# Performance work log

Measured on AMD Instinct MI355X. Metric: run time of the kernel, lower is better.

The kernel has to match this reference:

```python
import jax, jax.numpy as jnp
import numpy as np

B, S, E, H = 4, 2048, 1024, 16
D = E // H
EPS = 1e-5
NEG = -1e9


def setup_inputs() -> dict:
    key = jax.random.key(0)
    ks = jax.random.split(key, 16)
    scale = 1.0 / np.sqrt(E)
    inp = {
        "q": jax.random.normal(ks[0], (B, S, E), jnp.float32),
        "k": jax.random.normal(ks[1], (B, S, E), jnp.float32),
        "v": jax.random.normal(ks[2], (B, S, E), jnp.float32),
        "mask": jax.random.randint(ks[3], (B, S, S), 0, 2).astype(bool),
        # Linear weights stored as (in, out); matches torch math with random init.
        "W1": jax.random.normal(ks[4], (E, E), jnp.float32) * scale,
        "b1": jnp.zeros((E,), jnp.float32),
        "W2": jax.random.normal(ks[5], (E, E), jnp.float32) * scale,
        "b2": jnp.zeros((E,), jnp.float32),
        "W3": jax.random.normal(ks[6], (E, E), jnp.float32) * scale,
        "b3": jnp.zeros((E,), jnp.float32),
        "W4": jax.random.normal(ks[7], (E, E), jnp.float32) * scale,
        "b4": jnp.zeros((E,), jnp.float32),
        "gamma": jnp.ones((E,), jnp.float32),
        "beta": jnp.zeros((E,), jnp.float32),
    }
    return inp


def _layer_norm(x, gamma, beta):
    mu = jnp.mean(x, axis=-1, keepdims=True)
    var = jnp.mean(jnp.square(x - mu), axis=-1, keepdims=True)
    return (x - mu) * jax.lax.rsqrt(var + EPS) * gamma + beta


def reference(q, k, v, mask, W1, b1, W2, b2, W3, b3, W4, b4, gamma, beta):
    vn = _layer_norm(v, gamma, beta)          # same LayerNorm params used twice
    residual = vn
    # projections -> [B, H, S, D]
    qh = (q @ W1 + b1).reshape(B, S, H, D).transpose(0, 2, 1, 3)
    kh = (k @ W2 + b2).reshape(B, S, H, D).transpose(0, 2, 1, 3)
    vh = (vn @ W3 + b3).reshape(B, S, H, D).transpose(0, 2, 1, 3)
    # NOTE: original module omits the 1/sqrt(D) scale -- keep it faithful.
    scores = jnp.einsum("bhqd,bhkd->bhqk", qh, kh)
    scores = jnp.where(mask[:, None, :, :], NEG, scores)
    attn = jax.nn.softmax(scores, axis=-1)
    out = jnp.einsum("bhqk,bhkd->bhqd", attn, vh)
    out = out.transpose(0, 2, 1, 3).reshape(B, S, E)
    out = out @ W4 + b4 + residual
    return _layer_norm(out, gamma, beta)
```

## Files before the change

### kernel.cpp

```cpp
#include <hip/hip_runtime.h>

typedef unsigned short u16;
typedef unsigned int u32;
typedef unsigned long long u64;
typedef float f32x4 __attribute__((ext_vector_type(4)));
typedef short short8 __attribute__((ext_vector_type(8)));
typedef short bf16x4 __attribute__((ext_vector_type(4)));

#define BB 4
#define SS 2048
#define EE 1024
#define HH 16
#define DD 64
#define EPSV 1e-5f
#define LOG2E 1.4426950408889634f

__device__ __forceinline__ u16 f2b(float x) {
  u32 u = __float_as_uint(x);
  u32 r = (u + 0x7fffu + ((u >> 16) & 1u)) >> 16;
  return (u16)r;
}
__device__ __forceinline__ float b2f(u16 u) {
  return __uint_as_float(((u32)u) << 16);
}
__device__ __forceinline__ u32 cvtpk(float lo, float hi) {
  u32 r;
  asm("v_cvt_pk_bf16_f32 %0, %1, %2" : "=v"(r) : "v"(lo), "v"(hi));
  return r;
}
__device__ __forceinline__ float fexp2(float x) {
  float r;
  asm("v_exp_f32 %0, %1" : "=v"(r) : "v"(x));
  return r;
}
__device__ __forceinline__ void gload16(const void* g, void* l) {
  __builtin_amdgcn_global_load_lds(
      (const __attribute__((address_space(1))) u32*)g,
      (__attribute__((address_space(3))) u32*)l, 16, 0, 0);
}
__device__ __forceinline__ f32x4 mfma16(bf16x4 a, bf16x4 b, f32x4 c) {
#if __has_builtin(__builtin_amdgcn_mfma_f32_16x16x16_bf16)
  return __builtin_amdgcn_mfma_f32_16x16x16_bf16(a, b, c, 0, 0, 0);
#elif __has_builtin(__builtin_amdgcn_mfma_f32_16x16x16bf16_1k)
  return __builtin_amdgcn_mfma_f32_16x16x16bf16_1k(a, b, c, 0, 0, 0);
#else
  asm("v_mfma_f32_16x16x16_bf16 %0, %1, %2, %3"
      : "=v"(c) : "v"(a), "v"(b), "v"(c));
  return c;
#endif
}

template<bool OUT_BF16>
__global__ __launch_bounds__(256) void ln_kernel(const float* __restrict__ x,
    const float* __restrict__ gamma, const float* __restrict__ beta,
    void* __restrict__ outp) {
  int row = blockIdx.x;
  int t = threadIdx.x;
  const float4* xr = (const float4*)(x + (size_t)row * EE);
  float4 v = xr[t];
  float s = v.x + v.y + v.z + v.w;
  #pragma unroll
  for (int o = 1; o < 64; o <<= 1) s += __shfl_xor(s, o);
  __shared__ float red[8];
  int wid = t >> 6;
  if ((t & 63) == 0) red[wid] = s;
  __syncthreads();
  float mean = (red[0] + red[1] + red[2] + red[3]) * (1.0f / EE);
  float d0 = v.x - mean, d1 = v.y - mean, d2 = v.z - mean, d3 = v.w - mean;
  float sq = d0 * d0 + d1 * d1 + d2 * d2 + d3 * d3;
  #pragma unroll
  for (int o = 1; o < 64; o <<= 1) sq += __shfl_xor(sq, o);
  if ((t & 63) == 0) red[4 + wid] = sq;
  __syncthreads();
  float var = (red[4] + red[5] + red[6] + red[7]) * (1.0f / EE);
  float rstd = rsqrtf(var + EPSV);
  float4 g = ((const float4*)gamma)[t];
  float4 be = ((const float4*)beta)[t];
  float o0 = d0 * rstd * g.x + be.x;
  float o1 = d1 * rstd * g.y + be.y;
  float o2 = d2 * rstd * g.z + be.z;
  float o3 = d3 * rstd * g.w + be.w;
  if (OUT_BF16) {
    ushort4 pk;
    pk.x = f2b(o0); pk.y = f2b(o1); pk.z = f2b(o2); pk.w = f2b(o3);
    *(ushort4*)((u16*)outp + (size_t)row * EE + t * 4) = pk;
  } else {
    ((float4*)((float*)outp + (size_t)row * EE))[t] = make_float4(o0, o1, o2, o3);
  }
}

__global__ __launch_bounds__(256) void pre_kernel(
    const float* __restrict__ v, const float* __restrict__ gamma,
    const float* __restrict__ beta, u16* __restrict__ vn,
    const float* __restrict__ q, u16* __restrict__ qbf,
    const float* __restrict__ k, u16* __restrict__ kbf,
    const int* __restrict__ mask, u64* __restrict__ mp,
    const float* __restrict__ W1, const float* __restrict__ W2,
    const float* __restrict__ W3, const float* __restrict__ W4,
    u16* __restrict__ W1t, u16* __restrict__ W2t,
    u16* __restrict__ W3t, u16* __restrict__ W4t) {
  __shared__ float tile[32][33];
  __shared__ float red[8];
  int idx = blockIdx.x;
  int t = threadIdx.x;
  if (idx < 8192) {
    int row = idx;
    float4 vv = ((const float4*)(v + (size_t)row * EE))[t];
    float s = vv.x + vv.y + vv.z + vv.w;
    #pragma unroll
    for (int o = 1; o < 64; o <<= 1) s += __shfl_xor(s, o);
    int wid = t >> 6;
    if ((t & 63) == 0) red[wid] = s;
    __syncthreads();
    float mean = (red[0] + red[1] + red[2] + red[3]) * (1.0f / EE);
    float d0 = vv.x - mean, d1 = vv.y - mean, d2 = vv.z - mean, d3 = vv.w - mean;
    float sq = d0 * d0 + d1 * d1 + d2 * d2 + d3 * d3;
    #pragma unroll
    for (int o = 1; o < 64; o <<= 1) sq += __shfl_xor(sq, o);
    if ((t & 63) == 0) red[4 + wid] = sq;
    __syncthreads();
    float var = (red[4] + red[5] + red[6] + red[7]) * (1.0f / EE);
    float rstd = rsqrtf(var + EPSV);
    float4 g = ((const float4*)gamma)[t];
    float4 be = ((const float4*)beta)[t];
    ushort4 pk;
    pk.x = f2b(d0 * rstd * g.x + be.x);
    pk.y = f2b(d1 * rstd * g.y + be.y);
    pk.z = f2b(d2 * rstd * g.z + be.z);
    pk.w = f2b(d3 * rstd * g.w + be.w);
    *(ushort4*)(vn + (size_t)row * EE + t * 4) = pk;
  } else if (idx < 16384) {
    int i = idx - 8192;
    const float* x = (i >= 4096) ? k : q;
    u16* y = (i >= 4096) ? kbf : qbf;
    size_t off = ((size_t)(i & 4095) * 256 + t) * 8;
    float4 a = *(const float4*)(x + off);
    float4 c = *(const float4*)(x + off + 4);
    uint4 pk;
    pk.x = (u32)f2b(a.x) | ((u32)f2b(a.y) << 16);
    pk.y = (u32)f2b(a.z) | ((u32)f2b(a.w) << 16);
    pk.z = (u32)f2b(c.x) | ((u32)f2b(c.y) << 16);
    pk.w = (u32)f2b(c.z) | ((u32)f2b(c.w) << 16);
    *(uint4*)(y + off) = pk;
  } else if (idx < 32768) {
    int widx = idx - 16384;
    int wv = t >> 6, lane = t & 63;
    size_t base = (size_t)widx * 1024 + wv * 256;
    int v0 = mask[base + 0 * 64 + lane];
    int v1 = mask[base + 1 * 64 + lane];
    int v2 = mask[base + 2 * 64 + lane];
    int v3 = mask[base + 3 * 64 + lane];
    u64 b0 = __ballot(v0 != 0);
    u64 b1 = __ballot(v1 != 0);
    u64 b2 = __ballot(v2 != 0);
    u64 b3 = __ballot(v3 != 0);
    if (lane == 0) {
      u64* dst = &mp[base >> 6];
      dst[0] = b0; dst[1] = b1; dst[2] = b2; dst[3] = b3;
    }
  } else {
    int s = idx - 32768;
    int w = s >> 10, t2 = s & 1023;
    int kb = (t2 & 31) * 32, nb = (t2 >> 5) * 32;
    const float* W = (w == 0) ? W1 : (w == 1) ? W2 : (w == 2) ? W3 : W4;
    u16* Wt = (w == 0) ? W1t : (w == 1) ? W2t : (w == 2) ? W3t : W4t;
    int r = t >> 3, c = (t & 7) * 4;
    float4 vv = *(const float4*)&W[(size_t)(kb + r) * EE + nb + c];
    tile[r][c] = vv.x; tile[r][c + 1] = vv.y;
    tile[r][c + 2] = vv.z; tile[r][c + 3] = vv.w;
    __syncthreads();
    uint2 val;
    val.x = (u32)f2b(tile[c][r]) | ((u32)f2b(tile[c + 1][r]) << 16);
    val.y = (u32)f2b(tile[c + 2][r]) | ((u32)f2b(tile[c + 3][r]) << 16);
    *(uint2*)&Wt[(size_t)(nb + r) * EE + kb + c] = val;
  }
}

__global__ __launch_bounds__(256) void gemm_proj(
    const u16* __restrict__ Aq, const u16* __restrict__ Ak,
    const u16* __restrict__ Av,
    const u16* __restrict__ W1t, const u16* __restrict__ W2t,
    const u16* __restrict__ W3t,
    const float* __restrict__ b1, const float* __restrict__ b2,
    const float* __restrict__ b3,
    u16* __restrict__ qh, u16* __restrict__ kh, u16* __restrict__ vt,
    int yoff) {
  constexpr int N = 1024, K = 1024;
  __shared__ u16 Al[128 * 32];
  __shared__ u16 Bl[128 * 32];
  int y = blockIdx.y + yoff;
  int sel = y >> 6, my = y & 63;
  const u16* Ap = (sel == 0) ? Aq : (sel == 1) ? Ak : Av;
  const u16* Bt = (sel == 0) ? W1t : (sel == 1) ? W2t : W3t;
  const float* bias = (sel == 0) ? b1 : (sel == 1) ? b2 : b3;
  u16* Cp = (sel == 0) ? qh : (sel == 1) ? kh : vt;
  float oscale = (sel == 0) ? LOG2E : 1.0f;

  int t = threadIdx.x;
  int lane = t & 63, wid = t >> 6;
  int mb = my * 128, nb = blockIdx.x * 128;
  int wm = (wid >> 1) * 64, wn = (wid & 1) * 64;
  int l15 = lane & 15, lg = lane >> 4;

  int srow = lane >> 2;
  int schunk = (lane & 3) ^ (srow & 3);
  const u16* Ag = Ap + (size_t)(mb + wid * 32 + srow) * K + schunk * 8;
  const u16* Bg = Bt + (size_t)(nb + wid * 32 + srow) * K + schunk * 8;
  u16* Alw0 = &Al[(wid * 32) * 32];
  u16* Alw1 = &Al[(wid * 32 + 16) * 32];
  u16* Blw0 = &Bl[(wid * 32) * 32];
  u16* Blw1 = &Bl[(wid * 32 + 16) * 32];
  int ca = (lg ^ (l15 & 3)) * 8;

  f32x4 acc[4][4] = {};
  for (int kt = 0; kt < K; kt += 32) {
    gload16(Ag + kt, Alw0);
    gload16(Ag + kt + (size_t)16 * K, Alw1);
    gload16(Bg + kt, Blw0);
    gload16(Bg + kt + (size_t)16 * K, Blw1);
    __syncthreads();
    short8 af[4], bfv[4];
    #pragma unroll
    for (int mf = 0; mf < 4; mf++)
      af[mf] = *(const short8*)&Al[(wm + mf * 16 + l15) * 32 + ca];
    #pragma unroll
    for (int nf = 0; nf < 4; nf++)
      bfv[nf] = *(const short8*)&Bl[(wn + nf * 16 + l15) * 32 + ca];
    #pragma unroll
    for (int mf = 0; mf < 4; mf++)
      #pragma unroll
      for (int nf = 0; nf < 4; nf++)
        acc[mf][nf] = __builtin_amdgcn_mfma_f32_16x16x32_bf16(af[mf], bfv[nf], acc[mf][nf], 0, 0, 0);
    __syncthreads();
  }
  float bv[4];
  #pragma unroll
  for (int nf = 0; nf < 4; nf++) bv[nf] = bias[nb + wn + nf * 16 + l15];
  if (sel == 2) {
    #pragma unroll
    for (int mf = 0; mf < 4; mf++) {
      int m0 = mb + wm + mf * 16 + lg * 4;
      int bq = m0 >> 11, s0 = m0 & 2047;
      #pragma unroll
      for (int nf = 0; nf < 4; nf++) {
        int n = nb + wn + nf * 16 + l15;
        int h = n >> 6, d = n & 63;
        ushort4 pk;
        pk.x = f2b(acc[mf][nf][0] + bv[nf]);
        pk.y = f2b(acc[mf][nf][1] + bv[nf]);
        pk.z = f2b(acc[mf][nf][2] + bv[nf]);
        pk.w = f2b(acc[mf][nf][3] + bv[nf]);
        *(ushort4*)&vt[((size_t)((bq * HH + h) * DD + d)) * SS + s0] = pk;
      }
    }
  } else {
    #pragma unroll
    for (int mf = 0; mf < 4; mf++) {
      #pragma unroll
      for (int r = 0; r < 4; r++) {
        int m = mb + wm + mf * 16 + lg * 4 + r;
        #pragma unroll
        for (int nf = 0; nf < 4; nf++) {
          int n = nb + wn + nf * 16 + l15;
          Cp[(size_t)m * N + n] = f2b((acc[mf][nf][r] + bv[nf]) * oscale);
        }
      }
    }
  }
}

__global__ __launch_bounds__(256) void gemm_out(const u16* __restrict__ Ap,
    const u16* __restrict__ Bt, const float* __restrict__ bias,
    const u16* __restrict__ resid, float* __restrict__ Cp) {
  constexpr int N = 1024, K = 1024;
  __shared__ u16 Al[128 * 32];
  __shared__ u16 Bl[128 * 32];
  int t = threadIdx.x;
  int lane = t & 63, wid = t >> 6;
  int mb = blockIdx.y * 128, nb = blockIdx.x * 128;
  int wm = (wid >> 1) * 64, wn = (wid & 1) * 64;
  int l15 = lane & 15, lg = lane >> 4;
  int srow = lane >> 2;
  int schunk = (lane & 3) ^ (srow & 3);
  const u16* Ag = Ap + (size_t)(mb + wid * 32 + srow) * K + schunk * 8;
  const u16* Bg = Bt + (size_t)(nb + wid * 32 + srow) * K + schunk * 8;
  u16* Alw0 = &Al[(wid * 32) * 32];
  u16* Alw1 = &Al[(wid * 32 + 16) * 32];
  u16* Blw0 = &Bl[(wid * 32) * 32];
  u16* Blw1 = &Bl[(wid * 32 + 16) * 32];
  int ca = (lg ^ (l15 & 3)) * 8;
  f32x4 acc[4][4] = {};
  for (int kt = 0; kt < K; kt += 32) {
    gload16(Ag + kt, Alw0);
    gload16(Ag + kt + (size_t)16 * K, Alw1);
    gload16(Bg + kt, Blw0);
    gload16(Bg + kt + (size_t)16 * K, Blw1);
    __syncthreads();
    short8 af[4], bfv[4];
    #pragma unroll
    for (int mf = 0; mf < 4; mf++)
      af[mf] = *(const short8*)&Al[(wm + mf * 16 + l15) * 32 + ca];
    #pragma unroll
    for (int nf = 0; nf < 4; nf++)
      bfv[nf] = *(const short8*)&Bl[(wn + nf * 16 + l15) * 32 + ca];
    #pragma unroll
    for (int mf = 0; mf < 4; mf++)
      #pragma unroll
      for (int nf = 0; nf < 4; nf++)
        acc[mf][nf] = __builtin_amdgcn_mfma_f32_16x16x32_bf16(af[mf], bfv[nf], acc[mf][nf], 0, 0, 0);
    __syncthreads();
  }
  float bv[4];
  #pragma unroll
  for (int nf = 0; nf < 4; nf++) bv[nf] = bias[nb + wn + nf * 16 + l15];
  #pragma unroll
  for (int mf = 0; mf < 4; mf++) {
    #pragma unroll
    for (int r = 0; r < 4; r++) {
      int m = mb + wm + mf * 16 + lg * 4 + r;
      #pragma unroll
      for (int nf = 0; nf < 4; nf++) {
        int n = nb + wn + nf * 16 + l15;
        float rv = b2f(resid[(size_t)m * N + n]);
        Cp[(size_t)m * N + n] = acc[mf][nf][r] + bv[nf] + rv;
      }
    }
  }
}

__global__ __launch_bounds__(256) void attn_kernel(const u16* __restrict__ qh,
    const u16* __restrict__ kh, const u16* __restrict__ vt,
    const u64* __restrict__ mp, u16* __restrict__ outp) {
  __shared__ u16 Kl[64 * 64];
  __shared__ u16 Vl[64 * 64];
  __shared__ u64 lutq[16];
  int t = threadIdx.x, lane = t & 63, wid = t >> 6;
  int bh = blockIdx.x, b = bh >> 4, h = bh & 15;
  int qt = blockIdx.y;
  int l15 = lane & 15, lg = lane >> 4;

  if (t < 16) {
    u32 n = t;
    u32 w0 = ((n & 1) ? 0u : 0xFFFFu) | ((n & 2) ? 0u : 0xFFFF0000u);
    u32 w1 = ((n & 4) ? 0u : 0xFFFFu) | ((n & 8) ? 0u : 0xFFFF0000u);
    lutq[n] = (u64)w0 | ((u64)w1 << 32);
  }

  int qrow0 = qt * 128 + wid * 16 + l15;
  int qrow1 = qrow0 + 64;
  const u16* qbase0 = qh + ((size_t)(b * SS + qrow0)) * EE + h * DD;
  const u16* qbase1 = qh + ((size_t)(b * SS + qrow1)) * EE + h * DD;
  short8 qa0 = *(const short8*)(qbase0 + lg * 8);
  short8 qa1 = *(const short8*)(qbase0 + 32 + lg * 8);
  short8 qb0 = *(const short8*)(qbase1 + lg * 8);
  short8 qb1 = *(const short8*)(qbase1 + 32 + lg * 8);
  const u64* mrow0 = mp + (size_t)(b * SS + qrow0) * (SS / 64);
  const u64* mrow1 = mp + (size_t)(b * SS + qrow1) * (SS / 64);

  bf16x4 onesv;
  #pragma unroll
  for (int i = 0; i < 4; i++) onesv[i] = (short)0x3F80;

  int r0 = wid * 16 + (lane >> 3);
  int r1 = r0 + 8;
  int cc = lane & 7;
  int wk0 = r0 * 64 + ((cc ^ (r0 & 7)) * 8);
  int wk1 = r1 * 64 + ((cc ^ (r1 & 7)) * 8);
  const u16* kgb = kh + ((size_t)b * SS) * EE + h * DD;
  const u16* vgb = vt + ((size_t)bh * DD) * SS;

  int ck0 = (lg ^ (l15 & 7)) * 8;
  int ck1 = ((4 + lg) ^ (l15 & 7)) * 8;
  int vbase0 = l15 * 64 + ((lg >> 1) ^ (l15 & 7)) * 8 + (lg & 1) * 4;

  f32x4 Oa[4] = {}, Ob[4] = {};
  f32x4 asuma = {}, asumb = {};
  constexpr int NT = SS / 64;

  uint4 sk0 = *(const uint4*)(kgb + (size_t)r0 * EE + cc * 8);
  uint4 sk1 = *(const uint4*)(kgb + (size_t)r1 * EE + cc * 8);
  uint4 sv0 = *(const uint4*)(vgb + (size_t)r0 * SS + cc * 8);
  uint4 sv1 = *(const uint4*)(vgb + (size_t)r1 * SS + cc * 8);
  const u16* kp0 = kgb + (size_t)(64 + r0) * EE + cc * 8;
  const u16* kp1 = kgb + (size_t)(64 + r1) * EE + cc * 8;
  const u16* vp0 = vgb + (size_t)r0 * SS + 64 + cc * 8;
  const u16* vp1 = vgb + (size_t)r1 * SS + 64 + cc * 8;
  u64 mwa = mrow0[0];
  u64 mwb = mrow1[0];

  for (int kt = 0; kt < NT; ++kt) {
    *(uint4*)&Kl[wk0] = sk0;
    *(uint4*)&Kl[wk1] = sk1;
    *(uint4*)&Vl[wk0] = sv0;
    *(uint4*)&Vl[wk1] = sv1;
    __syncthreads();

    sk0 = *(const uint4*)kp0; kp0 += 64 * EE;
    sk1 = *(const uint4*)kp1; kp1 += 64 * EE;
    sv0 = *(const uint4*)vp0; vp0 += 64;
    sv1 = *(const uint4*)vp1; vp1 += 64;
    u64 mwan = mrow0[kt + 1];
    u64 mwbn = mrow1[kt + 1];

    u32 mloa = (u32)(mwa >> (lg * 4));
    u32 mhia = (u32)(mwa >> 32 >> (lg * 4));
    u32 mlob = (u32)(mwb >> (lg * 4));
    u32 mhib = (u32)(mwb >> 32 >> (lg * 4));
    uint2 pata[4], patb[4];
    pata[0] = *(uint2*)&lutq[mloa & 15u];
    pata[1] = *(uint2*)&lutq[(mloa >> 16) & 15u];
    pata[2] = *(uint2*)&lutq[mhia & 15u];
    pata[3] = *(uint2*)&lutq[(mhia >> 16) & 15u];
    patb[0] = *(uint2*)&lutq[mlob & 15u];
    patb[1] = *(uint2*)&lutq[(mlob >> 16) & 15u];
    patb[2] = *(uint2*)&lutq[mhib & 15u];
    patb[3] = *(uint2*)&lutq[(mhib >> 16) & 15u];

    f32x4 sca[4], scb[4];
    #pragma unroll
    for (int nf = 0; nf < 4; nf++) {
      int row = nf * 16 + l15;
      short8 k0 = *(const short8*)&Kl[row * 64 + ck0];
      short8 k1 = *(const short8*)&Kl[row * 64 + ck1];
      f32x4 za = {}, zb = {};
      za = __builtin_amdgcn_mfma_f32_16x16x32_bf16(k0, qa0, za, 0, 0, 0);
      za = __builtin_amdgcn_mfma_f32_16x16x32_bf16(k1, qa1, za, 0, 0, 0);
      zb = __builtin_amdgcn_mfma_f32_16x16x32_bf16(k0, qb0, zb, 0, 0, 0);
      zb = __builtin_amdgcn_mfma_f32_16x16x32_bf16(k1, qb1, zb, 0, 0, 0);
      sca[nf] = za;
      scb[nf] = zb;
    }

    #pragma unroll
    for (int nf = 0; nf < 4; nf++) {
      #pragma unroll
      for (int r = 0; r < 4; r++) {
        sca[nf][r] = fexp2(sca[nf][r]);
        scb[nf][r] = fexp2(scb[nf][r]);
      }
    }

    #pragma unroll
    for (int nf = 0; nf < 4; nf++) {
      bf16x4 pba, pbb;
      ((u32*)&pba)[0] = cvtpk(sca[nf][0], sca[nf][1]) & pata[nf].x;
      ((u32*)&pba)[1] = cvtpk(sca[nf][2], sca[nf][3]) & pata[nf].y;
      ((u32*)&pbb)[0] = cvtpk(scb[nf][0], scb[nf][1]) & patb[nf].x;
      ((u32*)&pbb)[1] = cvtpk(scb[nf][2], scb[nf][3]) & patb[nf].y;
      asuma = mfma16(onesv, pba, asuma);
      asumb = mfma16(onesv, pbb, asumb);
      int vo = vbase0 ^ (nf * 16);
      #pragma unroll
      for (int df = 0; df < 4; df++) {
        bf16x4 vf = *(const bf16x4*)&Vl[vo + df * 1024];
        Oa[df] = mfma16(vf, pba, Oa[df]);
        Ob[df] = mfma16(vf, pbb, Ob[df]);
      }
    }
    mwa = mwan;
    mwb = mwbn;
    __syncthreads();
  }

  float inva = 1.0f / asuma[0];
  float invb = 1.0f / asumb[0];
  u16* ob0 = outp + ((size_t)(b * SS + qrow0)) * EE + h * DD + lg * 4;
  u16* ob1 = outp + ((size_t)(b * SS + qrow1)) * EE + h * DD + lg * 4;
  #pragma unroll
  for (int df = 0; df < 4; df++) {
    ushort4 pka, pkb;
    pka.x = f2b(Oa[df][0] * inva);
    pka.y = f2b(Oa[df][1] * inva);
    pka.z = f2b(Oa[df][2] * inva);
    pka.w = f2b(Oa[df][3] * inva);
    pkb.x = f2b(Ob[df][0] * invb);
    pkb.y = f2b(Ob[df][1] * invb);
    pkb.z = f2b(Ob[df][2] * invb);
    pkb.w = f2b(Ob[df][3] * invb);
    *(ushort4*)(ob0 + df * 16) = pka;
    *(ushort4*)(ob1 + df * 16) = pkb;
  }
}

extern "C" void kernel_launch(void* const* d_in, const int* in_sizes, int n_in,
                              void* d_out, int out_size, void* d_ws, size_t ws_size,
                              hipStream_t stream) {
  (void)in_sizes; (void)n_in; (void)out_size;
  const float* q    = (const float*)d_in[0];
  const float* k    = (const float*)d_in[1];
  const float* v    = (const float*)d_in[2];
  const int*   mask = (const int*)d_in[3];
  const float* W1   = (const float*)d_in[4];
  const float* b1   = (const float*)d_in[5];
  const float* W2   = (const float*)d_in[6];
  const float* b2   = (const float*)d_in[7];
  const float* W3   = (const float*)d_in[8];
  const float* b3   = (const float*)d_in[9];
  const float* W4   = (const float*)d_in[10];
  const float* b4   = (const float*)d_in[11];
  const float* gamma = (const float*)d_in[12];
  const float* beta  = (const float*)d_in[13];
  float* out = (float*)d_out;
  char* ws = (char*)d_ws;
  const size_t MB = 1024 * 1024;
  u16* qh  = (u16*)(ws + 0 * MB);
  u16* kh  = (u16*)(ws + 16 * MB);
  u16* vt  = (u16*)(ws + 32 * MB);
  u16* ao  = (u16*)(ws + 48 * MB);
  u16* vn  = (u16*)(ws + 64 * MB);
  u16* W1t = (u16*)(ws + 80 * MB);
  u16* W2t = (u16*)(ws + 82 * MB);
  u16* W3t = (u16*)(ws + 84 * MB);
  u16* W4t = (u16*)(ws + 86 * MB);
  u64* mp  = (u64*)(ws + 88 * MB);
  float* tmp = (float*)(ws + 0 * MB);
  u16* qbf = ao;

  bool ws_ok = ws_size >= 107 * MB;
  u16* kbf = ws_ok ? (u16*)(ws + 90 * MB) : vt;

  pre_kernel<<<36864, 256, 0, stream>>>(v, gamma, beta, vn, q, qbf, k, kbf,
                                        mask, mp, W1, W2, W3, W4,
                                        W1t, W2t, W3t, W4t);
  if (ws_ok) {
    gemm_proj<<<dim3(8, 192), 256, 0, stream>>>(qbf, kbf, vn, W1t, W2t, W3t,
                                                b1, b2, b3, qh, kh, vt, 0);
  } else {
    gemm_proj<<<dim3(8, 128), 256, 0, stream>>>(qbf, kbf, vn, W1t, W2t, W3t,
                                                b1, b2, b3, qh, kh, vt, 0);
    gemm_proj<<<dim3(8, 64), 256, 0, stream>>>(qbf, kbf, vn, W1t, W2t, W3t,
                                               b1, b2, b3, qh, kh, vt, 128);
  }
  attn_kernel<<<dim3(64, 16), 256, 0, stream>>>(qh, kh, vt, mp, ao);
  gemm_out<<<dim3(8, 64), 256, 0, stream>>>(ao, W4t, b4, vn, tmp);
  ln_kernel<false><<<8192, 256, 0, stream>>>(tmp, gamma, beta, out);
}
```

Measured before the change: 280.9 us.

## Double-buffer K/V tiles in attention and swap GEMM grid axes

The attention kernel now keeps two LDS buffers for K and V. The next tile is written into the spare buffer while the current one is consumed, which removes one barrier per iteration and lets the LDS stores overlap the score MFMAs. The projection and output GEMMs also swap grid dimensions so that consecutive blocks walk along M while sharing a weight column tile, which changes the L2 reuse pattern. This doubles attention LDS use to about 32KB and may lower occupancy.

```diff
diff --git a/kernel.cpp b/kernel.cpp
--- a/kernel.cpp
+++ b/kernel.cpp
@@ -188,7 +188,7 @@
   constexpr int N = 1024, K = 1024;
   __shared__ u16 Al[128 * 32];
   __shared__ u16 Bl[128 * 32];
-  int y = blockIdx.y + yoff;
+  int y = blockIdx.x + yoff;
   int sel = y >> 6, my = y & 63;
   const u16* Ap = (sel == 0) ? Aq : (sel == 1) ? Ak : Av;
   const u16* Bt = (sel == 0) ? W1t : (sel == 1) ? W2t : W3t;
@@ -198,7 +198,7 @@
 
   int t = threadIdx.x;
   int lane = t & 63, wid = t >> 6;
-  int mb = my * 128, nb = blockIdx.x * 128;
+  int mb = my * 128, nb = blockIdx.y * 128;
   int wm = (wid >> 1) * 64, wn = (wid & 1) * 64;
   int l15 = lane & 15, lg = lane >> 4;
 
@@ -277,7 +277,7 @@
   __shared__ u16 Bl[128 * 32];
   int t = threadIdx.x;
   int lane = t & 63, wid = t >> 6;
-  int mb = blockIdx.y * 128, nb = blockIdx.x * 128;
+  int mb = blockIdx.x * 128, nb = blockIdx.y * 128;
   int wm = (wid >> 1) * 64, wn = (wid & 1) * 64;
   int l15 = lane & 15, lg = lane >> 4;
   int srow = lane >> 2;
@@ -331,8 +331,8 @@
 __global__ __launch_bounds__(256) void attn_kernel(const u16* __restrict__ qh,
     const u16* __restrict__ kh, const u16* __restrict__ vt,
     const u64* __restrict__ mp, u16* __restrict__ outp) {
-  __shared__ u16 Kl[64 * 64];
-  __shared__ u16 Vl[64 * 64];
+  __shared__ u16 Kl[2][64 * 64];
+  __shared__ u16 Vl[2][64 * 64];
   __shared__ u64 lutq[16];
   int t = threadIdx.x, lane = t & 63, wid = t >> 6;
   int bh = blockIdx.x, b = bh >> 4, h = bh & 15;
@@ -381,26 +381,29 @@
   uint4 sk1 = *(const uint4*)(kgb + (size_t)r1 * EE + cc * 8);
   uint4 sv0 = *(const uint4*)(vgb + (size_t)r0 * SS + cc * 8);
   uint4 sv1 = *(const uint4*)(vgb + (size_t)r1 * SS + cc * 8);
+  *(uint4*)&Kl[0][wk0] = sk0;
+  *(uint4*)&Kl[0][wk1] = sk1;
+  *(uint4*)&Vl[0][wk0] = sv0;
+  *(uint4*)&Vl[0][wk1] = sv1;
   const u16* kp0 = kgb + (size_t)(64 + r0) * EE + cc * 8;
   const u16* kp1 = kgb + (size_t)(64 + r1) * EE + cc * 8;
   const u16* vp0 = vgb + (size_t)r0 * SS + 64 + cc * 8;
   const u16* vp1 = vgb + (size_t)r1 * SS + 64 + cc * 8;
   u64 mwa = mrow0[0];
   u64 mwb = mrow1[0];
-
+  __syncthreads();
+
+  int cur = 0;
   for (int kt = 0; kt < NT; ++kt) {
-    *(uint4*)&Kl[wk0] = sk0;
-    *(uint4*)&Kl[wk1] = sk1;
-    *(uint4*)&Vl[wk0] = sv0;
-    *(uint4*)&Vl[wk1] = sv1;
-    __syncthreads();
-
     sk0 = *(const uint4*)kp0; kp0 += 64 * EE;
     sk1 = *(const uint4*)kp1; kp1 += 64 * EE;
     sv0 = *(const uint4*)vp0; vp0 += 64;
     sv1 = *(const uint4*)vp1; vp1 += 64;
     u64 mwan = mrow0[kt + 1];
     u64 mwbn = mrow1[kt + 1];
+
+    const u16* Kc = Kl[cur];
+    const u16* Vc = Vl[cur];
 
     u32 mloa = (u32)(mwa >> (lg * 4));
     u32 mhia = (u32)(mwa >> 32 >> (lg * 4));
@@ -420,8 +423,8 @@
     #pragma unroll
     for (int nf = 0; nf < 4; nf++) {
       int row = nf * 16 + l15;
-      short8 k0 = *(const short8*)&Kl[row * 64 + ck0];
-      short8 k1 = *(const short8*)&Kl[row * 64 + ck1];
+      short8 k0 = *(const short8*)&Kc[row * 64 + ck0];
+      short8 k1 = *(const short8*)&Kc[row * 64 + ck1];
       f32x4 za = {}, zb = {};
       za = __builtin_amdgcn_mfma_f32_16x16x32_bf16(k0, qa0, za, 0, 0, 0);
       za = __builtin_amdgcn_mfma_f32_16x16x32_bf16(k1, qa1, za, 0, 0, 0);
@@ -438,6 +441,15 @@
         sca[nf][r] = fexp2(sca[nf][r]);
         scb[nf][r] = fexp2(scb[nf][r]);
       }
+    }
+
+    {
+      u16* Kn = Kl[cur ^ 1];
+      u16* Vn = Vl[cur ^ 1];
+      *(uint4*)&Kn[wk0] = sk0;
+      *(uint4*)&Kn[wk1] = sk1;
+      *(uint4*)&Vn[wk0] = sv0;
+      *(uint4*)&Vn[wk1] = sv1;
     }
 
     #pragma unroll
@@ -452,7 +464,7 @@
       int vo = vbase0 ^ (nf * 16);
       #pragma unroll
       for (int df = 0; df < 4; df++) {
-        bf16x4 vf = *(const bf16x4*)&Vl[vo + df * 1024];
+        bf16x4 vf = *(const bf16x4*)&Vc[vo + df * 1024];
         Oa[df] = mfma16(vf, pba, Oa[df]);
         Ob[df] = mfma16(vf, pbb, Ob[df]);
       }
@@ -460,6 +472,7 @@
     mwa = mwan;
     mwb = mwbn;
     __syncthreads();
+    cur ^= 1;
   }
 
   float inva = 1.0f / asuma[0];
@@ -523,15 +536,15 @@
                                         mask, mp, W1, W2, W3, W4,
                                         W1t, W2t, W3t, W4t);
   if (ws_ok) {
-    gemm_proj<<<dim3(8, 192), 256, 0, stream>>>(qbf, kbf, vn, W1t, W2t, W3t,
+    gemm_proj<<<dim3(192, 8), 256, 0, stream>>>(qbf, kbf, vn, W1t, W2t, W3t,
                                                 b1, b2, b3, qh, kh, vt, 0);
   } else {
-    gemm_proj<<<dim3(8, 128), 256, 0, stream>>>(qbf, kbf, vn, W1t, W2t, W3t,
+    gemm_proj<<<dim3(128, 8), 256, 0, stream>>>(qbf, kbf, vn, W1t, W2t, W3t,
                                                 b1, b2, b3, qh, kh, vt, 0);
-    gemm_proj<<<dim3(8, 64), 256, 0, stream>>>(qbf, kbf, vn, W1t, W2t, W3t,
+    gemm_proj<<<dim3(64, 8), 256, 0, stream>>>(qbf, kbf, vn, W1t, W2t, W3t,
                                                b1, b2, b3, qh, kh, vt, 128);
   }
   attn_kernel<<<dim3(64, 16), 256, 0, stream>>>(qh, kh, vt, mp, ao);
-  gemm_out<<<dim3(8, 64), 256, 0, stream>>>(ao, W4t, b4, vn, tmp);
+  gemm_out<<<dim3(64, 8), 256, 0, stream>>>(ao, W4t, b4, vn, tmp);
   ln_kernel<false><<<8192, 256, 0, stream>>>(tmp, gamma, beta, out);
 }
```

Result: no change. 282.7 us (+0.6%).
